# Kernel optimization log

Measured on AMD Instinct MI355X. Metric: run time of the kernel, lower is better.

## Reference

```python
import jax, jax.numpy as jnp
import numpy as np


def setup_inputs() -> dict:
    key = jax.random.key(0)
    k1, k2, k3 = jax.random.split(key, 3)
    B, C, H, W = 32, 768, 32, 32
    Cr = 192  # max(1, C // 4)
    x = jax.random.normal(k1, (B, C, H, W), dtype=jnp.float32)
    # 1x1 conv weights flattened to dense matrices (kernel is 1x1)
    w1 = jax.random.normal(k2, (Cr, C), dtype=jnp.float32) * (1.0 / np.sqrt(C))
    b1 = jnp.zeros((Cr,), dtype=jnp.float32)
    w2 = jax.random.normal(k3, (C, Cr), dtype=jnp.float32) * (1.0 / np.sqrt(Cr))
    b2 = jnp.zeros((C,), dtype=jnp.float32)
    return {"x": x, "w1": w1, "b1": b1, "w2": w2, "b2": b2}


def reference(x, w1, b1, w2, b2):
    # Squeeze: global average pool over spatial dims -> [B, C]
    s = jnp.mean(x, axis=(2, 3))
    # Excitation: tiny MLP with swish then sigmoid gate
    h = s @ w1.T + b1                    # [B, Cr]
    h = h * jax.nn.sigmoid(h)            # swish
    g = jax.nn.sigmoid(h @ w2.T + b2)    # [B, C]
    # Scale: broadcast multiply back over the full feature map
    return x * g[:, :, None, None]
```

## Files before the change

### kernel.cpp

```cpp
#include <hip/hip_runtime.h>
#include <math.h>

#define Bn 32
#define Cn 768
#define CRn 192
#define HWn 1024

__global__ __launch_bounds__(256) void se_mean(const float* __restrict__ x,
                                               float* __restrict__ s) {
    const int bc = blockIdx.x;
    const float4* xp = (const float4*)(x + (size_t)bc * HWn);
    float4 v = xp[threadIdx.x];
    float sum = v.x + v.y + v.z + v.w;
    #pragma unroll
    for (int off = 32; off > 0; off >>= 1) sum += __shfl_down(sum, off);
    __shared__ float part[4];
    const int lane = threadIdx.x & 63;
    const int wid  = threadIdx.x >> 6;
    if (lane == 0) part[wid] = sum;
    __syncthreads();
    if (threadIdx.x == 0) {
        s[bc] = (part[0] + part[1] + part[2] + part[3]) * (1.0f / (float)HWn);
    }
}

__global__ __launch_bounds__(256) void se_mlp(const float* __restrict__ s,
                                              const float* __restrict__ w1,
                                              const float* __restrict__ b1,
                                              const float* __restrict__ w2,
                                              const float* __restrict__ b2,
                                              float* __restrict__ g) {
    const int b = blockIdx.x;
    __shared__ __align__(16) float sl[Cn];
    __shared__ __align__(16) float hl[CRn];

    for (int i = threadIdx.x; i < Cn; i += 256) sl[i] = s[b * Cn + i];
    __syncthreads();

    if (threadIdx.x < CRn) {
        const int j = threadIdx.x;
        const float4* wr = (const float4*)(w1 + (size_t)j * Cn);
        const float4* sp = (const float4*)sl;
        float acc = 0.0f;
        #pragma unroll 4
        for (int k = 0; k < Cn / 4; ++k) {
            float4 wv = wr[k];
            float4 sv = sp[k];
            acc += wv.x * sv.x + wv.y * sv.y + wv.z * sv.z + wv.w * sv.w;
        }
        acc += b1[j];
        hl[j] = acc / (1.0f + expf(-acc));
    }
    __syncthreads();

    for (int j = threadIdx.x; j < Cn; j += 256) {
        const float4* wr = (const float4*)(w2 + (size_t)j * CRn);
        const float4* hp = (const float4*)hl;
        float acc = 0.0f;
        #pragma unroll 4
        for (int k = 0; k < CRn / 4; ++k) {
            float4 wv = wr[k];
            float4 hv = hp[k];
            acc += wv.x * hv.x + wv.y * hv.y + wv.z * hv.z + wv.w * hv.w;
        }
        acc += b2[j];
        g[b * Cn + j] = 1.0f / (1.0f + expf(-acc));
    }
}

__global__ __launch_bounds__(256) void se_scale(const float* __restrict__ x,
                                                const float* __restrict__ g,
                                                float* __restrict__ out) {
    const int bc = blockIdx.x;
    const float gv = g[bc];
    const float4* xp = (const float4*)(x + (size_t)bc * HWn);
    float4* op = (float4*)(out + (size_t)bc * HWn);
    float4 v = xp[threadIdx.x];
    v.x *= gv; v.y *= gv; v.z *= gv; v.w *= gv;
    op[threadIdx.x] = v;
}

extern "C" void kernel_launch(void* const* d_in, const int* in_sizes, int n_in,
                              void* d_out, int out_size, void* d_ws, size_t ws_size,
                              hipStream_t stream) {
    const float* x  = (const float*)d_in[0];
    const float* w1 = (const float*)d_in[1];
    const float* b1 = (const float*)d_in[2];
    const float* w2 = (const float*)d_in[3];
    const float* b2 = (const float*)d_in[4];
    float* out = (float*)d_out;

    float* s = (float*)d_ws;
    float* g = s + (size_t)Bn * Cn;

    se_mean <<<Bn * Cn, 256, 0, stream>>>(x, s);
    se_mlp  <<<Bn,      256, 0, stream>>>(s, w1, b1, w2, b2, g);
    se_scale<<<Bn * Cn, 256, 0, stream>>>(x, g, out);
}
```

Measured before the change: 238.1 us.

## Parallelize SE MLP across wavefronts and fuse gate computation into scale kernel

The first MLP layer moves from one block per batch to one wavefront per (batch, hidden unit), with a wave-level shuffle reduction, so many more CUs share the work. The second layer and sigmoid gate are now computed inside the scale kernel, one 64-lane dot product per (b,c) block, which drops the separate gate pass and its write and read of g. The old se_mlp ran on only 32 blocks and serialized long dot products, which likely made it a bottleneck. In exchange, each scale block adds a barrier and a small reduction before its store.

```diff
diff --git a/kernel.cpp b/kernel.cpp
--- a/kernel.cpp
+++ b/kernel.cpp
@@ -24,58 +24,64 @@
     }
 }
 
-__global__ __launch_bounds__(256) void se_mlp(const float* __restrict__ s,
-                                              const float* __restrict__ w1,
-                                              const float* __restrict__ b1,
-                                              const float* __restrict__ w2,
-                                              const float* __restrict__ b2,
-                                              float* __restrict__ g) {
-    const int b = blockIdx.x;
-    __shared__ __align__(16) float sl[Cn];
-    __shared__ __align__(16) float hl[CRn];
+__global__ __launch_bounds__(256) void se_h(const float* __restrict__ s,
+                                            const float* __restrict__ w1,
+                                            const float* __restrict__ b1,
+                                            float* __restrict__ h) {
+    const int wid  = threadIdx.x >> 6;
+    const int lane = threadIdx.x & 63;
+    const int b = blockIdx.x / (CRn / 4);
+    const int j = (blockIdx.x % (CRn / 4)) * 4 + wid;
 
-    for (int i = threadIdx.x; i < Cn; i += 256) sl[i] = s[b * Cn + i];
-    __syncthreads();
-
-    if (threadIdx.x < CRn) {
-        const int j = threadIdx.x;
-        const float4* wr = (const float4*)(w1 + (size_t)j * Cn);
-        const float4* sp = (const float4*)sl;
-        float acc = 0.0f;
-        #pragma unroll 4
-        for (int k = 0; k < Cn / 4; ++k) {
-            float4 wv = wr[k];
-            float4 sv = sp[k];
-            acc += wv.x * sv.x + wv.y * sv.y + wv.z * sv.z + wv.w * sv.w;
-        }
-        acc += b1[j];
-        hl[j] = acc / (1.0f + expf(-acc));
+    const float4* wr = (const float4*)(w1 + (size_t)j * Cn);
+    const float4* sp = (const float4*)(s + (size_t)b * Cn);
+    float acc = 0.0f;
+    #pragma unroll
+    for (int t = 0; t < 3; ++t) {
+        float4 wv = wr[lane + 64 * t];
+        float4 sv = sp[lane + 64 * t];
+        acc += wv.x * sv.x + wv.y * sv.y + wv.z * sv.z + wv.w * sv.w;
     }
-    __syncthreads();
-
-    for (int j = threadIdx.x; j < Cn; j += 256) {
-        const float4* wr = (const float4*)(w2 + (size_t)j * CRn);
-        const float4* hp = (const float4*)hl;
-        float acc = 0.0f;
-        #pragma unroll 4
-        for (int k = 0; k < CRn / 4; ++k) {
-            float4 wv = wr[k];
-            float4 hv = hp[k];
-            acc += wv.x * hv.x + wv.y * hv.y + wv.z * hv.z + wv.w * hv.w;
-        }
-        acc += b2[j];
-        g[b * Cn + j] = 1.0f / (1.0f + expf(-acc));
+    #pragma unroll
+    for (int off = 32; off > 0; off >>= 1) acc += __shfl_down(acc, off);
+    if (lane == 0) {
+        float v = acc + b1[j];
+        h[b * CRn + j] = v / (1.0f + expf(-v));
     }
 }
 
-__global__ __launch_bounds__(256) void se_scale(const float* __restrict__ x,
-                                                const float* __restrict__ g,
-                                                float* __restrict__ out) {
+__global__ __launch_bounds__(256) void se_scale_g(const float* __restrict__ x,
+                                                  const float* __restrict__ h,
+                                                  const float* __restrict__ w2,
+                                                  const float* __restrict__ b2,
+                                                  float* __restrict__ out) {
     const int bc = blockIdx.x;
-    const float gv = g[bc];
+    const int b = bc / Cn;
+    const int c = bc % Cn;
+
     const float4* xp = (const float4*)(x + (size_t)bc * HWn);
     float4* op = (float4*)(out + (size_t)bc * HWn);
     float4 v = xp[threadIdx.x];
+
+    __shared__ float gs;
+    if (threadIdx.x < 64) {
+        const int lane = threadIdx.x;
+        const float* hp = h  + (size_t)b * CRn;
+        const float* wp = w2 + (size_t)c * CRn;
+        float acc = 0.0f;
+        #pragma unroll
+        for (int t = 0; t < 3; ++t) {
+            acc += hp[lane + 64 * t] * wp[lane + 64 * t];
+        }
+        #pragma unroll
+        for (int off = 32; off > 0; off >>= 1) acc += __shfl_down(acc, off);
+        if (lane == 0) {
+            float z = acc + b2[c];
+            gs = 1.0f / (1.0f + expf(-z));
+        }
+    }
+    __syncthreads();
+    const float gv = gs;
     v.x *= gv; v.y *= gv; v.z *= gv; v.w *= gv;
     op[threadIdx.x] = v;
 }
@@ -91,9 +97,9 @@
     float* out = (float*)d_out;
 
     float* s = (float*)d_ws;
-    float* g = s + (size_t)Bn * Cn;
+    float* h = s + (size_t)Bn * Cn;
 
-    se_mean <<<Bn * Cn, 256, 0, stream>>>(x, s);
-    se_mlp  <<<Bn,      256, 0, stream>>>(s, w1, b1, w2, b2, g);
-    se_scale<<<Bn * Cn, 256, 0, stream>>>(x, g, out);
+    se_mean   <<<Bn * Cn,        256, 0, stream>>>(x, s);
+    se_h      <<<Bn * (CRn / 4), 256, 0, stream>>>(s, w1, b1, h);
+    se_scale_g<<<Bn * Cn,        256, 0, stream>>>(x, h, w2, b2, out);
 }
```

Measured after the change: 195.4 us. 17.9% less time.
